# Kernel optimization log

Measured on AMD Instinct MI355X. Metric: run time of the kernel, lower is better.

The kernel has to match this reference:

```python
import jax, jax.numpy as jnp
import numpy as np

NUM_HEAD = 16
D_MODEL = 1024


def setup_inputs() -> dict:
    key = jax.random.key(0)
    ks = jax.random.split(key, 11)
    B, S, D = 2, 2048, D_MODEL
    scale = 1.0 / np.sqrt(D)
    inp = {
        "q": jax.random.normal(ks[0], (B, S, D), dtype=jnp.float32),
        "k": jax.random.normal(ks[1], (B, S, D), dtype=jnp.float32),
        "v": jax.random.normal(ks[2], (B, S, D), dtype=jnp.float32),
        "Wq": jax.random.normal(ks[3], (D, D), dtype=jnp.float32) * scale,
        "bq": jnp.zeros((D,), dtype=jnp.float32),
        "Wk": jax.random.normal(ks[4], (D, D), dtype=jnp.float32) * scale,
        "bk": jnp.zeros((D,), dtype=jnp.float32),
        "Wv": jax.random.normal(ks[5], (D, D), dtype=jnp.float32) * scale,
        "bv": jnp.zeros((D,), dtype=jnp.float32),
        "Wo": jax.random.normal(ks[6], (D, D), dtype=jnp.float32) * scale,
        "bo": jnp.zeros((D,), dtype=jnp.float32),
    }
    return inp


def _split_heads(x, num_head):
    B, S, D = x.shape
    return x.reshape(B, S, num_head, D // num_head).transpose(0, 2, 1, 3)  # [B,H,S,d]


def reference(q, k, v, Wq, bq, Wk, bk, Wv, bv, Wo, bo):
    H = NUM_HEAD
    qp = q @ Wq + bq
    kp = k @ Wk + bk  # computed but UNUSED, matching source bug
    vp = v @ Wv + bv
    # source bug: k := split_heads(v-projection)
    qh = _split_heads(qp, H)          # [B,H,S,d]
    kh = _split_heads(vp, H)          # [B,H,S,d]  (v-projection used as keys)
    vh = _split_heads(vp, H)          # [B,H,S,d]
    d = qh.shape[-1]
    scores = jnp.einsum('bhqd,bhkd->bhqk', qh, kh) / jnp.sqrt(jnp.asarray(d, qh.dtype))
    attn = jax.nn.softmax(scores, axis=-1)
    out = jnp.einsum('bhqk,bhkd->bhqd', attn, vh)  # [B,H,S,d]
    B, _, S, _ = out.shape
    out = out.transpose(0, 2, 1, 3).reshape(B, S, H * d)
    return out @ Wo + bo
```

## Files before the change

kernel.cpp:

```cpp
#include <hip/hip_runtime.h>
#include <hip/hip_bf16.h>

using bfrag  = __attribute__((ext_vector_type(8))) __bf16;
using f32x4  = __attribute__((ext_vector_type(4))) float;
using f32x16 = __attribute__((ext_vector_type(16))) float;
using v4u    = __attribute__((ext_vector_type(4))) unsigned int;
using v2u    = __attribute__((ext_vector_type(2))) unsigned int;

__device__ __forceinline__ ushort f2bf(float f) {
    union { float f; unsigned u; } c; c.f = f;
    return (ushort)((c.u + 0x7fffu + ((c.u >> 16) & 1u)) >> 16);
}

__device__ __forceinline__ float bf2f(ushort u) {
    union { unsigned u; float f; } c; c.u = (unsigned)u << 16; return c.f;
}

__device__ __forceinline__ unsigned pack_bf16x2(float lo, float hi) {
    union { __hip_bfloat162 h; unsigned u; } c;
    c.h = __float22bfloat162_rn(make_float2(lo, hi));
    return c.u;
}

__device__ __forceinline__ void gld_lds16(const ushort* g, ushort* l) {
    __builtin_amdgcn_global_load_lds(
        (const __attribute__((address_space(1))) void*)g,
        (__attribute__((address_space(3))) void*)l, 16, 0, 0);
}

__device__ __forceinline__ f32x16 mfma32(bfrag a, bfrag b, f32x16 c) {
    return __builtin_amdgcn_mfma_f32_32x32x16_bf16(a, b, c, 0, 0, 0);
}


__global__ void cvt_bf16_2(const float* __restrict__ a, ushort* __restrict__ da,
                           const float* __restrict__ b, ushort* __restrict__ db, int n4) {
    int i = blockIdx.x * blockDim.x + threadIdx.x;
    const float* s; ushort* d;
    if (i < n4) { s = a; d = da; } else { s = b; d = db; i -= n4; }
    float4 f = ((const float4*)s)[i];
    ((ushort4*)d)[i] = make_ushort4(f2bf(f.x), f2bf(f.y), f2bf(f.z), f2bf(f.w));
}

__global__ void cvt_T3(const float* __restrict__ s0, ushort* __restrict__ d0,
                       const float* __restrict__ s1, ushort* __restrict__ d1,
                       const float* __restrict__ s2, ushort* __restrict__ d2) {
    __shared__ float t[32][33];
    const int z = blockIdx.z;
    const float* src = z == 0 ? s0 : z == 1 ? s1 : s2;
    ushort* dst = z == 0 ? d0 : z == 1 ? d1 : d2;
    const int tx = threadIdx.x, ty = threadIdx.y;
    const int c0 = blockIdx.x * 32, r0 = blockIdx.y * 32;
    for (int i = ty; i < 32; i += 8) t[i][tx] = src[(size_t)(r0 + i) * 1024 + c0 + tx];
    __syncthreads();
    for (int i = ty; i < 32; i += 8) dst[(size_t)(c0 + i) * 1024 + r0 + tx] = f2bf(t[tx][i]);
}


__global__ __launch_bounds__(256) void vpt_T(const ushort* __restrict__ VPb, ushort* __restrict__ VPT) {
    __shared__ ushort T[64][72];
    const int st = blockIdx.x, bh = blockIdx.y;
    const int b = bh >> 4, h = bh & 15;
    const int tid = threadIdx.x;
#pragma unroll
    for (int i = 0; i < 2; ++i) {
        const int c = tid + i * 256;
        const int row = c >> 3, col8 = (c & 7) * 8;
        v4u d = *(const v4u*)(VPb + (size_t)(b * 2048 + st * 64 + row) * 1024 + h * 64 + col8);
        *(v4u*)&T[row][col8] = d;
    }
    __syncthreads();
    const int d = tid >> 2, sch = tid & 3;
    union { ushort s[16]; v4u v[2]; } tmp;
#pragma unroll
    for (int j = 0; j < 16; ++j) {
        const int js = (j & 3) | ((j >> 1) & 4) | ((j << 1) & 8);
        tmp.s[j] = T[sch * 16 + js][d];
    }
    ushort* dst = VPT + ((size_t)bh * 64 + d) * 2048 + st * 64 + sch * 16;
    *(v4u*)dst = tmp.v[0];
    *(v4u*)(dst + 8) = tmp.v[1];
}


template<bool BF16OUT>
__device__ __forceinline__ void gemm_body(
    const ushort* __restrict__ A, const ushort* __restrict__ Bt,
    const float* __restrict__ bias, void* __restrict__ Cout,
    float scale, int bM, int bN)
{
    __shared__ ushort As[2][128 * 32];
    __shared__ ushort Bs[2][128 * 32];
    const int tid = threadIdx.x;
    const int lane = tid & 63, w = tid >> 6;
    const int l15 = lane & 15, lg = lane >> 4;
    const int wr = w >> 1, wc = w & 1;

    const ushort* Ag = A + (size_t)bM * 128 * 1024;
    const ushort* Bg = Bt + (size_t)bN * 128 * 1024;
    const int r0 = w * 32 + (lane >> 2);
    const int cc = (lane & 3) * 8;

    auto STAGE = [&](int buf, int kt) {
        const int kk = kt * 32;
#pragma unroll
        for (int i = 0; i < 2; ++i) {
            const int row = r0 + i * 16;
            const int c = w * 2 + i;
            gld_lds16(Ag + (size_t)row * 1024 + kk + cc, &As[buf][c * 512]);
            gld_lds16(Bg + (size_t)row * 1024 + kk + cc, &Bs[buf][c * 512]);
        }
    };

    f32x4 acc[4][4];
#pragma unroll
    for (int m = 0; m < 4; ++m)
#pragma unroll
        for (int n = 0; n < 4; ++n) acc[m][n] = (f32x4){0.f, 0.f, 0.f, 0.f};

    STAGE(0, 0);
    __syncthreads();
    int cur = 0;
    for (int kt = 0; kt < 32; ++kt) {
        if (kt < 31) STAGE(cur ^ 1, kt + 1);
        bfrag aF[4], bF[4];
#pragma unroll
        for (int m = 0; m < 4; ++m) aF[m] = *(const bfrag*)&As[cur][(wr * 64 + m * 16 + l15) * 32 + lg * 8];
#pragma unroll
        for (int n = 0; n < 4; ++n) bF[n] = *(const bfrag*)&Bs[cur][(wc * 64 + n * 16 + l15) * 32 + lg * 8];
        __builtin_amdgcn_s_setprio(1);
#pragma unroll
        for (int m = 0; m < 4; ++m)
#pragma unroll
            for (int n = 0; n < 4; ++n)
                acc[m][n] = __builtin_amdgcn_mfma_f32_16x16x32_bf16(aF[m], bF[n], acc[m][n], 0, 0, 0);
        __builtin_amdgcn_s_setprio(0);
        if (kt < 31) {
            __syncthreads();
            cur ^= 1;
        }
    }

#pragma unroll
    for (int m = 0; m < 4; ++m)
#pragma unroll
        for (int n = 0; n < 4; ++n) {
            const int gcol = bN * 128 + wc * 64 + n * 16 + l15;
            const float bv = bias[gcol];
#pragma unroll
            for (int j = 0; j < 4; ++j) {
                const int grow = bM * 128 + wr * 64 + m * 16 + lg * 4 + j;
                const float val = (acc[m][n][j] + bv) * scale;
                if constexpr (BF16OUT) {
                    ((ushort*)Cout)[(size_t)grow * 1024 + gcol] = f2bf(val);
                } else {
                    ((float*)Cout)[(size_t)grow * 1024 + gcol] = val;
                }
            }
        }
}

__global__ __launch_bounds__(256) void gemm_qv(
    const ushort* __restrict__ Aq, const ushort* __restrict__ Wq, const float* __restrict__ bq, ushort* __restrict__ Cq,
    const ushort* __restrict__ Av, const ushort* __restrict__ Wv, const float* __restrict__ bv, ushort* __restrict__ Cv,
    float qscale)
{
    const int z = blockIdx.z;
    gemm_body<true>(z ? Av : Aq, z ? Wv : Wq, z ? bv : bq, z ? (void*)Cv : (void*)Cq,
                    z ? 1.0f : qscale, blockIdx.y, blockIdx.x);
}

__global__ __launch_bounds__(256) void gemm_o(
    const ushort* __restrict__ A, const ushort* __restrict__ Bt,
    const float* __restrict__ bias, float* __restrict__ Cout)
{
    gemm_body<false>(A, Bt, bias, Cout, 1.0f, blockIdx.y, blockIdx.x);
}


__global__ __launch_bounds__(256, 2) void attn_kernel(
    const ushort* __restrict__ QP, const ushort* __restrict__ VP,
    const ushort* __restrict__ VPT, ushort* __restrict__ Opart, float* __restrict__ Lpart)
{
    __shared__ ushort Ks[2][4096];
    __shared__ ushort Vs[2][4096];
    const int tid = threadIdx.x;
    const int w = tid >> 6, lane = tid & 63;
    const int l31 = lane & 31, hi = lane >> 5;
    const int bh = blockIdx.x, qt = blockIdx.y, half = blockIdx.z;
    const int b = bh >> 4, h = bh & 15;
    const int qrow0 = qt * 256 + w * 64;
    const int k0 = half * 16;

    const int sr = lane >> 3;
    const int sc = ((lane & 7) ^ sr) * 8;
    const ushort* Kg = VP + (size_t)(b * 2048) * 1024 + h * 64 + sc;
    const ushort* Vg = VPT + (size_t)bh * 131072 + sc;

    auto STAGE = [&](int slot, int kt) {
#pragma unroll
        for (int i = 0; i < 2; ++i) {
            const int kb = w * 2 + i;
            const int r = kb * 8 + sr;
            gld_lds16(Kg + (size_t)(kt * 64 + r) * 1024, &Ks[slot][kb * 512]);
            gld_lds16(Vg + (size_t)r * 2048 + kt * 64, &Vs[slot][kb * 512]);
        }
    };

    const ushort* Qp = QP + ((size_t)(b * 2048 + qrow0 + l31)) * 1024 + h * 64 + hi * 8;
    bfrag qA[4], qBt[4];
#pragma unroll
    for (int ds = 0; ds < 4; ++ds) {
        qA[ds]  = *(const bfrag*)(Qp + ds * 16);
        qBt[ds] = *(const bfrag*)(Qp + 32 * 1024 + ds * 16);
    }

    f32x16 OA0, OA1, OB0, OB1;
#pragma unroll
    for (int r = 0; r < 16; ++r) { OA0[r] = 0.f; OA1[r] = 0.f; OB0[r] = 0.f; OB1[r] = 0.f; }
    float lrunA = 0.f, lrunB = 0.f;

    const int swz = (l31 & 7) << 4;
    const int cA = hi * 16;

    STAGE(0, k0);
    __syncthreads();

    auto SOFTMAX = [&](f32x16& S0, f32x16& S1, bfrag (&pB)[4], float& lrun) {
        float p[32];
#pragma unroll
        for (int r = 0; r < 16; ++r) {
            p[r]      = __builtin_amdgcn_exp2f(S0[r]);
            p[16 + r] = __builtin_amdgcn_exp2f(S1[r]);
        }
        float s8[8];
#pragma unroll
        for (int i = 0; i < 8; ++i) s8[i] = (p[i] + p[i + 8]) + (p[i + 16] + p[i + 24]);
        lrun += ((s8[0] + s8[1]) + (s8[2] + s8[3])) + ((s8[4] + s8[5]) + (s8[6] + s8[7]));
#pragma unroll
        for (int c = 0; c < 4; ++c) {
            union { v4u u; bfrag f; } cv;
#pragma unroll
            for (int wd = 0; wd < 4; ++wd)
                cv.u[wd] = pack_bf16x2(p[8 * c + 2 * wd], p[8 * c + 2 * wd + 1]);
            pB[c] = cv.f;
        }
    };

#pragma unroll 1
    for (int t = 0; t < 16; ++t) {
        if (t > 0) __syncthreads();
        if (t + 1 < 16) STAGE((t + 1) & 1, k0 + t + 1);
        const ushort* Kb_ = Ks[t & 1];
        const ushort* Vb_ = Vs[t & 1];

        bfrag k0f[4], k1f[4];
#pragma unroll
        for (int ds = 0; ds < 4; ++ds) {
            k0f[ds] = *(const bfrag*)&Kb_[(l31 * 128 + ((ds * 32 + cA) ^ swz)) >> 1];
            k1f[ds] = *(const bfrag*)&Kb_[((l31 + 32) * 128 + ((ds * 32 + cA) ^ swz)) >> 1];
        }
        f32x16 SA0, SA1, SB0, SB1;
#pragma unroll
        for (int r = 0; r < 16; ++r) { SA0[r] = -16.f; SA1[r] = -16.f; SB0[r] = -16.f; SB1[r] = -16.f; }
        __builtin_amdgcn_s_setprio(1);
#pragma unroll
        for (int ds = 0; ds < 4; ++ds) {
            SA0 = mfma32(k0f[ds], qA[ds], SA0);
            SA1 = mfma32(k1f[ds], qA[ds], SA1);
            SB0 = mfma32(k0f[ds], qBt[ds], SB0);
            SB1 = mfma32(k1f[ds], qBt[ds], SB1);
        }
        __builtin_amdgcn_s_setprio(0);

        bfrag pBA[4], pBB[4];
        SOFTMAX(SA0, SA1, pBA, lrunA);
        SOFTMAX(SB0, SB1, pBB, lrunB);

        bfrag vF0[4], vF1[4];
#pragma unroll
        for (int c = 0; c < 4; ++c) {
            vF0[c] = *(const bfrag*)&Vb_[(l31 * 128 + ((c * 32 + cA) ^ swz)) >> 1];
            vF1[c] = *(const bfrag*)&Vb_[((l31 + 32) * 128 + ((c * 32 + cA) ^ swz)) >> 1];
        }
        __builtin_amdgcn_s_setprio(1);
#pragma unroll
        for (int c = 0; c < 4; ++c) {
            OA0 = mfma32(vF0[c], pBA[c], OA0);
            OA1 = mfma32(vF1[c], pBA[c], OA1);
            OB0 = mfma32(vF0[c], pBB[c], OB0);
            OB1 = mfma32(vF1[c], pBB[c], OB1);
        }
        __builtin_amdgcn_s_setprio(0);
    }

    lrunA += __shfl_xor(lrunA, 32);
    lrunB += __shfl_xor(lrunB, 32);
    ushort* AoA = Opart + (size_t)half * 4194304
                + (size_t)(b * 2048 + qrow0 + l31) * 1024 + h * 64 + hi * 4;
    ushort* AoB = AoA + 32 * 1024;
#pragma unroll
    for (int t = 0; t < 2; ++t) {
#pragma unroll
        for (int g = 0; g < 4; ++g) {
            const float a0 = t ? OA1[4 * g + 0] : OA0[4 * g + 0];
            const float a1 = t ? OA1[4 * g + 1] : OA0[4 * g + 1];
            const float a2 = t ? OA1[4 * g + 2] : OA0[4 * g + 2];
            const float a3 = t ? OA1[4 * g + 3] : OA0[4 * g + 3];
            *(v2u*)(AoA + t * 32 + g * 8) = (v2u){pack_bf16x2(a0, a1), pack_bf16x2(a2, a3)};
            const float b0 = t ? OB1[4 * g + 0] : OB0[4 * g + 0];
            const float b1 = t ? OB1[4 * g + 1] : OB0[4 * g + 1];
            const float b2 = t ? OB1[4 * g + 2] : OB0[4 * g + 2];
            const float b3 = t ? OB1[4 * g + 3] : OB0[4 * g + 3];
            *(v2u*)(AoB + t * 32 + g * 8) = (v2u){pack_bf16x2(b0, b1), pack_bf16x2(b2, b3)};
        }
    }
    if (hi == 0) {
        Lpart[half * 65536 + bh * 2048 + qrow0 + l31] = lrunA;
        Lpart[half * 65536 + bh * 2048 + qrow0 + 32 + l31] = lrunB;
    }
}


__global__ __launch_bounds__(256) void combine_kernel(
    const ushort* __restrict__ Opart, const float* __restrict__ Lpart,
    ushort* __restrict__ AO)
{
    const int t = blockIdx.x * 256 + threadIdx.x;
    const int e0 = t * 8;
    const int grow = e0 >> 10, col = e0 & 1023;
    const int b = grow >> 11, s = grow & 2047, h = col >> 6;
    const int li = (b * 16 + h) * 2048 + s;
    const float l = Lpart[li] + Lpart[65536 + li];
    const float inv = 1.0f / l;
    v4u a = *(const v4u*)(Opart + e0);
    v4u c = *(const v4u*)(Opart + 4194304 + e0);
    v4u o;
#pragma unroll
    for (int wd = 0; wd < 4; ++wd) {
        const float x0 = (bf2f((ushort)(a[wd] & 0xffff)) + bf2f((ushort)(c[wd] & 0xffff))) * inv;
        const float x1 = (bf2f((ushort)(a[wd] >> 16))    + bf2f((ushort)(c[wd] >> 16)))    * inv;
        o[wd] = pack_bf16x2(x0, x1);
    }
    *(v4u*)(AO + e0) = o;
}


extern "C" void kernel_launch(void* const* d_in, const int* in_sizes, int n_in,
                              void* d_out, int out_size, void* d_ws, size_t ws_size,
                              hipStream_t stream) {
    (void)in_sizes; (void)n_in; (void)out_size; (void)ws_size;
    const float* q  = (const float*)d_in[0];
    const float* v  = (const float*)d_in[2];
    const float* Wq = (const float*)d_in[3];
    const float* bq = (const float*)d_in[4];
    const float* Wv = (const float*)d_in[7];
    const float* bv = (const float*)d_in[8];
    const float* Wo = (const float*)d_in[9];
    const float* bo = (const float*)d_in[10];
    float* out = (float*)d_out;
    char* ws = (char*)d_ws;
    const size_t MB = 1ull << 20;
    ushort* qbf = (ushort*)(ws + 0);
    ushort* vbf = (ushort*)(ws + 8 * MB);
    ushort* WqT = (ushort*)(ws + 16 * MB);
    ushort* WvT = (ushort*)(ws + 18 * MB);
    ushort* WoT = (ushort*)(ws + 20 * MB);
    ushort* QPb = (ushort*)(ws + 22 * MB);
    ushort* VPb = (ushort*)(ws + 30 * MB);
    ushort* VPT = (ushort*)(ws + 38 * MB);

    ushort* Opart = (ushort*)(ws + 0);
    float*  Lpart = (float*)(ws + 16 * MB);
    ushort* AO    = QPb;

    cvt_bf16_2<<<8192, 256, 0, stream>>>(q, qbf, v, vbf, 1048576);
    cvt_T3<<<dim3(32, 32, 3), dim3(32, 8), 0, stream>>>(Wq, WqT, Wv, WvT, Wo, WoT);

    const float qscale = 0.125f * 1.44269504088896340736f;
    gemm_qv<<<dim3(8, 32, 2), 256, 0, stream>>>(qbf, WqT, bq, QPb,
                                                vbf, WvT, bv, VPb, qscale);
    vpt_T<<<dim3(32, 32), 256, 0, stream>>>(VPb, VPT);
    attn_kernel<<<dim3(32, 8, 2), 256, 0, stream>>>(QPb, VPb, VPT, Opart, Lpart);
    combine_kernel<<<2048, 256, 0, stream>>>(Opart, Lpart, AO);
    gemm_o<<<dim3(8, 32), 256, 0, stream>>>(AO, WoT, bo, out);
}
```

Measured before the change: 133.5 us.

## Halve GEMM M-tile to 64 rows and merge conversion kernels into one launch

The shared GEMM body now computes 64x128 tiles instead of 128x128, doubling the grid for the QV and output projections and raising launch bounds to 4 blocks per CU. This trades per-block data reuse for more blocks, giving better CU fill on a 4096-row GEMM (256 blocks previously). The two fp32-to-bf16 conversion kernels are merged into a single launch covering the weight transposes and the activation casts, which removes one kernel launch. The smaller tile re-reads the B operand more often, adding global and LDS traffic.

```diff
diff --git a/kernel.cpp b/kernel.cpp
--- a/kernel.cpp
+++ b/kernel.cpp
@@ -33,27 +33,29 @@
 }
 
 
-__global__ void cvt_bf16_2(const float* __restrict__ a, ushort* __restrict__ da,
-                           const float* __restrict__ b, ushort* __restrict__ db, int n4) {
-    int i = blockIdx.x * blockDim.x + threadIdx.x;
-    const float* s; ushort* d;
-    if (i < n4) { s = a; d = da; } else { s = b; d = db; i -= n4; }
-    float4 f = ((const float4*)s)[i];
-    ((ushort4*)d)[i] = make_ushort4(f2bf(f.x), f2bf(f.y), f2bf(f.z), f2bf(f.w));
-}
-
-__global__ void cvt_T3(const float* __restrict__ s0, ushort* __restrict__ d0,
-                       const float* __restrict__ s1, ushort* __restrict__ d1,
-                       const float* __restrict__ s2, ushort* __restrict__ d2) {
-    __shared__ float t[32][33];
+__global__ void cvt_all(const float* __restrict__ s0, ushort* __restrict__ d0,
+                        const float* __restrict__ s1, ushort* __restrict__ d1,
+                        const float* __restrict__ s2, ushort* __restrict__ d2,
+                        const float* __restrict__ q, ushort* __restrict__ qbf,
+                        const float* __restrict__ v, ushort* __restrict__ vbf) {
     const int z = blockIdx.z;
-    const float* src = z == 0 ? s0 : z == 1 ? s1 : s2;
-    ushort* dst = z == 0 ? d0 : z == 1 ? d1 : d2;
-    const int tx = threadIdx.x, ty = threadIdx.y;
-    const int c0 = blockIdx.x * 32, r0 = blockIdx.y * 32;
-    for (int i = ty; i < 32; i += 8) t[i][tx] = src[(size_t)(r0 + i) * 1024 + c0 + tx];
-    __syncthreads();
-    for (int i = ty; i < 32; i += 8) dst[(size_t)(c0 + i) * 1024 + r0 + tx] = f2bf(t[tx][i]);
+    if (z < 3) {
+        __shared__ float t[32][33];
+        const float* src = z == 0 ? s0 : z == 1 ? s1 : s2;
+        ushort* dst = z == 0 ? d0 : z == 1 ? d1 : d2;
+        const int tx = threadIdx.x, ty = threadIdx.y;
+        const int c0 = blockIdx.x * 32, r0 = blockIdx.y * 32;
+        for (int i = ty; i < 32; i += 8) t[i][tx] = src[(size_t)(r0 + i) * 1024 + c0 + tx];
+        __syncthreads();
+        for (int i = ty; i < 32; i += 8) dst[(size_t)(c0 + i) * 1024 + r0 + tx] = f2bf(t[tx][i]);
+    } else {
+        const int tid = threadIdx.y * 32 + threadIdx.x;
+        int i = ((z - 3) * 1024 + blockIdx.y * 32 + blockIdx.x) * 256 + tid;
+        const float* s; ushort* d;
+        if (i < 1048576) { s = q; d = qbf; } else { s = v; d = vbf; i -= 1048576; }
+        float4 f = ((const float4*)s)[i];
+        ((ushort4*)d)[i] = make_ushort4(f2bf(f.x), f2bf(f.y), f2bf(f.z), f2bf(f.w));
+    }
 }
 
 
@@ -89,32 +91,29 @@
     const float* __restrict__ bias, void* __restrict__ Cout,
     float scale, int bM, int bN)
 {
-    __shared__ ushort As[2][128 * 32];
+    __shared__ ushort As[2][64 * 32];
     __shared__ ushort Bs[2][128 * 32];
     const int tid = threadIdx.x;
     const int lane = tid & 63, w = tid >> 6;
     const int l15 = lane & 15, lg = lane >> 4;
     const int wr = w >> 1, wc = w & 1;
 
-    const ushort* Ag = A + (size_t)bM * 128 * 1024;
+    const ushort* Ag = A + (size_t)bM * 64 * 1024;
     const ushort* Bg = Bt + (size_t)bN * 128 * 1024;
-    const int r0 = w * 32 + (lane >> 2);
-    const int cc = (lane & 3) * 8;
+    const int ar = tid >> 2;
+    const int cc = (tid & 3) * 8;
 
     auto STAGE = [&](int buf, int kt) {
         const int kk = kt * 32;
-#pragma unroll
-        for (int i = 0; i < 2; ++i) {
-            const int row = r0 + i * 16;
-            const int c = w * 2 + i;
-            gld_lds16(Ag + (size_t)row * 1024 + kk + cc, &As[buf][c * 512]);
-            gld_lds16(Bg + (size_t)row * 1024 + kk + cc, &Bs[buf][c * 512]);
-        }
+        gld_lds16(Ag + (size_t)ar * 1024 + kk + cc, &As[buf][tid * 8]);
+#pragma unroll
+        for (int i = 0; i < 2; ++i)
+            gld_lds16(Bg + (size_t)(ar + i * 64) * 1024 + kk + cc, &Bs[buf][(tid + i * 256) * 8]);
     };
 
-    f32x4 acc[4][4];
-#pragma unroll
-    for (int m = 0; m < 4; ++m)
+    f32x4 acc[2][4];
+#pragma unroll
+    for (int m = 0; m < 2; ++m)
 #pragma unroll
         for (int n = 0; n < 4; ++n) acc[m][n] = (f32x4){0.f, 0.f, 0.f, 0.f};
 
@@ -123,14 +122,14 @@
     int cur = 0;
     for (int kt = 0; kt < 32; ++kt) {
         if (kt < 31) STAGE(cur ^ 1, kt + 1);
-        bfrag aF[4], bF[4];
-#pragma unroll
-        for (int m = 0; m < 4; ++m) aF[m] = *(const bfrag*)&As[cur][(wr * 64 + m * 16 + l15) * 32 + lg * 8];
+        bfrag aF[2], bF[4];
+#pragma unroll
+        for (int m = 0; m < 2; ++m) aF[m] = *(const bfrag*)&As[cur][(wr * 32 + m * 16 + l15) * 32 + lg * 8];
 #pragma unroll
         for (int n = 0; n < 4; ++n) bF[n] = *(const bfrag*)&Bs[cur][(wc * 64 + n * 16 + l15) * 32 + lg * 8];
         __builtin_amdgcn_s_setprio(1);
 #pragma unroll
-        for (int m = 0; m < 4; ++m)
+        for (int m = 0; m < 2; ++m)
 #pragma unroll
             for (int n = 0; n < 4; ++n)
                 acc[m][n] = __builtin_amdgcn_mfma_f32_16x16x32_bf16(aF[m], bF[n], acc[m][n], 0, 0, 0);
@@ -142,14 +141,14 @@
     }
 
 #pragma unroll
-    for (int m = 0; m < 4; ++m)
+    for (int m = 0; m < 2; ++m)
 #pragma unroll
         for (int n = 0; n < 4; ++n) {
             const int gcol = bN * 128 + wc * 64 + n * 16 + l15;
             const float bv = bias[gcol];
 #pragma unroll
             for (int j = 0; j < 4; ++j) {
-                const int grow = bM * 128 + wr * 64 + m * 16 + lg * 4 + j;
+                const int grow = bM * 64 + wr * 32 + m * 16 + lg * 4 + j;
                 const float val = (acc[m][n][j] + bv) * scale;
                 if constexpr (BF16OUT) {
                     ((ushort*)Cout)[(size_t)grow * 1024 + gcol] = f2bf(val);
@@ -160,7 +159,7 @@
         }
 }
 
-__global__ __launch_bounds__(256) void gemm_qv(
+__global__ __launch_bounds__(256, 4) void gemm_qv(
     const ushort* __restrict__ Aq, const ushort* __restrict__ Wq, const float* __restrict__ bq, ushort* __restrict__ Cq,
     const ushort* __restrict__ Av, const ushort* __restrict__ Wv, const float* __restrict__ bv, ushort* __restrict__ Cv,
     float qscale)
@@ -170,7 +169,7 @@
                     z ? 1.0f : qscale, blockIdx.y, blockIdx.x);
 }
 
-__global__ __launch_bounds__(256) void gemm_o(
+__global__ __launch_bounds__(256, 4) void gemm_o(
     const ushort* __restrict__ A, const ushort* __restrict__ Bt,
     const float* __restrict__ bias, float* __restrict__ Cout)
 {
@@ -374,14 +373,14 @@
     float*  Lpart = (float*)(ws + 16 * MB);
     ushort* AO    = QPb;
 
-    cvt_bf16_2<<<8192, 256, 0, stream>>>(q, qbf, v, vbf, 1048576);
-    cvt_T3<<<dim3(32, 32, 3), dim3(32, 8), 0, stream>>>(Wq, WqT, Wv, WvT, Wo, WoT);
+    cvt_all<<<dim3(32, 32, 11), dim3(32, 8), 0, stream>>>(
+        Wq, WqT, Wv, WvT, Wo, WoT, q, qbf, v, vbf);
 
     const float qscale = 0.125f * 1.44269504088896340736f;
-    gemm_qv<<<dim3(8, 32, 2), 256, 0, stream>>>(qbf, WqT, bq, QPb,
+    gemm_qv<<<dim3(8, 64, 2), 256, 0, stream>>>(qbf, WqT, bq, QPb,
                                                 vbf, WvT, bv, VPb, qscale);
     vpt_T<<<dim3(32, 32), 256, 0, stream>>>(VPb, VPT);
     attn_kernel<<<dim3(32, 8, 2), 256, 0, stream>>>(QPb, VPb, VPT, Opart, Lpart);
     combine_kernel<<<2048, 256, 0, stream>>>(Opart, Lpart, AO);
-    gemm_o<<<dim3(8, 32), 256, 0, stream>>>(AO, WoT, bo, out);
-}
+    gemm_o<<<dim3(8, 64), 256, 0, stream>>>(AO, WoT, bo, out);
+}
```

Measured after the change: 125.8 us. 5.8% less time.
